# Optimization experiments

Hardware: AMD Instinct MI355X
Metric: run time of the kernel (lower is better)

Reference implementation:

```python
import jax, jax.numpy as jnp
import numpy as np

N_NODES = 20000
DEG = 16
T_IN = 12
T_OUT = 24
N_HEADS = 4
N_CH = 4
BATCH = 2


def setup_inputs() -> dict:
    key = jax.random.key(0)
    k1, k2, k3, k4 = jax.random.split(key, 4)
    # unique directed edges: (i, (i+d) % N) for d in 1..DEG, plus self loops
    src = jnp.repeat(jnp.arange(N_NODES, dtype=jnp.int64), DEG)
    offs = jnp.tile(jnp.arange(1, DEG + 1, dtype=jnp.int64), N_NODES)
    dst = (src + offs) % N_NODES
    loops = jnp.arange(N_NODES, dtype=jnp.int64)
    d_edges = jnp.concatenate([
        jnp.stack([src, dst], axis=1),
        jnp.stack([loops, loops], axis=1),
    ], axis=0)  # (E, 2), E = N*DEG + N
    E = d_edges.shape[0]
    x = jax.random.normal(k1, (BATCH, T_IN, N_NODES, N_CH), dtype=jnp.float32)
    d_ew = jax.random.uniform(k2, (E, N_HEADS), dtype=jnp.float32)
    # shrink: Linear(t_in*n_heads -> T-t_in)
    fan_in = T_IN * N_HEADS
    bound = 1.0 / np.sqrt(fan_in)
    W = jax.random.uniform(k3, (T_OUT - T_IN, fan_in), minval=-bound, maxval=bound, dtype=jnp.float32)
    b = jax.random.uniform(k4, (T_OUT - T_IN,), minval=-bound, maxval=bound, dtype=jnp.float32)
    return {"x": x, "d_ew": d_ew, "W": W, "b": b, "d_edges": d_edges}


def reference(x, d_ew, W, b, d_edges):
    # x: (B, t, N, C); d_ew: (E, H); d_edges: (E, 2)
    node_i = d_edges[:, 0]
    node_j = d_edges[:, 1]
    B, t, N, C = x.shape
    # gather source node features per edge -> (E, B, t, C)
    x_src = jnp.moveaxis(x[:, :, node_i, :], 2, 0)
    # messages: (E, B, t, H, C)
    msg = d_ew[:, None, None, :, None] * x_src[:, :, :, None, :]
    # scatter-add into destination nodes (equivalent to the dense N x N holder sum)
    agg = jax.ops.segment_sum(msg, node_j, num_segments=N)  # (N, B, t, H, C)
    y = jnp.moveaxis(agg, 0, 2)                              # (B, t, N, H, C)
    # permute(0,2,4,1,3) -> (B, N, C, t, H), flatten (t, H)
    y = jnp.transpose(y, (0, 2, 4, 1, 3)).reshape(B, N, C, t * d_ew.shape[1])
    y = jax.nn.relu(jnp.einsum('bncf,of->bnco', y, W) + b)   # (B, N, C, T-t)
    y = jnp.transpose(y, (0, 3, 1, 2))                       # (B, T-t, N, C)
    return jnp.concatenate([x, y], axis=1)                   # (B, T, N, C)
```

## Files before the change

### kernel.cpp

```cpp
#include <hip/hip_runtime.h>

namespace {
constexpr int NN  = 20000;
constexpr int DEG = 16;
constexpr int TI  = 12;
constexpr int NB  = 2;
constexpr int ESELF  = NN * DEG;
constexpr int TILE   = 32;
constexpr int NTILES = NN / TILE;
constexpr int WN     = 48;
constexpr int EWP    = 68;
constexpr int REDP   = 13;
}

__device__ __forceinline__ void pk_fma(float2& d, float2 a, float2 b) {
    asm("v_pk_fma_f32 %0, %1, %2, %0" : "+v"(d) : "v"(a), "v"(b));
}
__device__ __forceinline__ void pk_fma_blo(float2& d, float2 a, float2 b) {
    asm("v_pk_fma_f32 %0, %1, %2, %0 op_sel:[0,0,0] op_sel_hi:[1,0,1]"
        : "+v"(d) : "v"(a), "v"(b));
}
__device__ __forceinline__ void pk_fma_bhi(float2& d, float2 a, float2 b) {
    asm("v_pk_fma_f32 %0, %1, %2, %0 op_sel:[0,1,0] op_sel_hi:[1,1,1]"
        : "+v"(d) : "v"(a), "v"(b));
}

__global__ __launch_bounds__(128) void gnn_fused(
    const float* __restrict__ x,
    const float* __restrict__ ew,
    const float* __restrict__ W,
    const float* __restrict__ bias,
    float* __restrict__ out)
{
    __shared__ float x_lds[TI * WN * 4];
    __shared__ float ew_lds[WN * EWP];
    __shared__ float ews[TILE * 4];
    __shared__ float red[TILE * 2 * REDP * 2];

    const int tid = threadIdx.x;
    const int bid = blockIdx.x;
    const int b   = bid / NTILES;
    const int n0  = (bid % NTILES) * TILE;

    {
        const float* xb = x + (size_t)b * TI * NN * 4;
#pragma unroll
        for (int i = 0; i < 5; ++i) {
            if (i < 4 || tid < 64) {
                const int idx4 = tid + 128 * i;
                const int t  = idx4 / WN;
                const int wi = idx4 - t * WN;
                int s = n0 - 16 + wi; s += (s >> 31) & NN;
                const float* src = xb + (size_t)(t * NN + s) * 4;
                float* dstbase = x_lds + (size_t)(128 * i + (tid & 64)) * 4;
                __builtin_amdgcn_global_load_lds(
                    (const __attribute__((address_space(1))) void*)src,
                    (__attribute__((address_space(3))) void*)dstbase, 16, 0, 0);
            }
        }
    }
    {
        const float4* ew4 = (const float4*)ew;
#pragma unroll
        for (int i = 0; i < 6; ++i) {
            const int idx = tid + 128 * i;
            const int sl = idx >> 4, r4 = idx & 15;
            int s = n0 - 16 + sl; s += (s >> 31) & NN;
            const float4 v = ew4[s * DEG + r4];
            *(float4*)&ew_lds[sl * EWP + r4 * 4] = v;
        }
        if (tid < TILE) ((float4*)ews)[tid] = ew4[ESELF + n0 + tid];
    }
    __syncthreads();

    const int c2 = tid & 1;
    const int nl = (tid >> 1) & 31;
    const int tg = tid >> 6;
    const int t0 = __builtin_amdgcn_readfirstlane(tg * 6);

    float2 agg[6][4] = {};

#pragma unroll
    for (int k = 0; k < DEG; ++k) {
        const int wi = nl + 15 - k;
        const float4 e4 = *(const float4*)&ew_lds[wi * EWP + 4 * k];
        const float2 e01 = {e4.x, e4.y}, e23 = {e4.z, e4.w};
#pragma unroll
        for (int j = 0; j < 6; ++j) {
            const float2 xv =
                *(const float2*)&x_lds[(t0 + j) * (WN * 4) + wi * 4 + c2 * 2];
            pk_fma_blo(agg[j][0], xv, e01);
            pk_fma_bhi(agg[j][1], xv, e01);
            pk_fma_blo(agg[j][2], xv, e23);
            pk_fma_bhi(agg[j][3], xv, e23);
        }
    }

    {
        const size_t ob = (size_t)b * 24 * NN * 4 + (size_t)(n0 + nl) * 4 + c2 * 2;
        const float2 e01 = *(const float2*)&ews[nl * 4 + 0];
        const float2 e23 = *(const float2*)&ews[nl * 4 + 2];
#pragma unroll
        for (int j = 0; j < 6; ++j) {
            const float2 xv =
                *(const float2*)&x_lds[(t0 + j) * (WN * 4) + (nl + 16) * 4 + c2 * 2];
            *(float2*)&out[ob + (size_t)(t0 + j) * NN * 4] = xv;
            pk_fma_blo(agg[j][0], xv, e01);
            pk_fma_bhi(agg[j][1], xv, e01);
            pk_fma_blo(agg[j][2], xv, e23);
            pk_fma_bhi(agg[j][3], xv, e23);
        }
    }

    float2 y2[12];
#pragma unroll
    for (int o = 0; o < 12; ++o) {
        float2 acc = {0.f, 0.f};
#pragma unroll
        for (int j = 0; j < 6; ++j) {
            const float* Wr = W + o * 48 + (t0 + j) * 4;
            acc.x = fmaf(Wr[0], agg[j][0].x, acc.x);
            acc.y = fmaf(Wr[0], agg[j][0].y, acc.y);
            acc.x = fmaf(Wr[1], agg[j][1].x, acc.x);
            acc.y = fmaf(Wr[1], agg[j][1].y, acc.y);
            acc.x = fmaf(Wr[2], agg[j][2].x, acc.x);
            acc.y = fmaf(Wr[2], agg[j][2].y, acc.y);
            acc.x = fmaf(Wr[3], agg[j][3].x, acc.x);
            acc.y = fmaf(Wr[3], agg[j][3].y, acc.y);
        }
        y2[o] = acc;
    }

    if (tg == 1) {
        float* r = red + (size_t)(nl * 2 + c2) * REDP * 2;
#pragma unroll
        for (int o = 0; o < 12; ++o) *(float2*)&r[o * 2] = y2[o];
    }
    __syncthreads();
    if (tg == 0) {
        const float* r = red + (size_t)(nl * 2 + c2) * REDP * 2;
        const size_t ob = (size_t)(b * 24 + 12) * NN * 4
                        + (size_t)(n0 + nl) * 4 + c2 * 2;
#pragma unroll
        for (int o = 0; o < 12; ++o) {
            const float2 p = *(const float2*)&r[o * 2];
            const float bo = bias[o];
            float2 v = {fmaxf(y2[o].x + p.x + bo, 0.f),
                        fmaxf(y2[o].y + p.y + bo, 0.f)};
            *(float2*)&out[ob + (size_t)o * NN * 4] = v;
        }
    }
}

extern "C" void kernel_launch(void* const* d_in, const int* in_sizes, int n_in,
                              void* d_out, int out_size, void* d_ws, size_t ws_size,
                              hipStream_t stream) {
    const float* x    = (const float*)d_in[0];
    const float* ew   = (const float*)d_in[1];
    const float* W    = (const float*)d_in[2];
    const float* bias = (const float*)d_in[3];
    float* out = (float*)d_out;

    const int blocks = NB * NTILES;
    hipLaunchKernelGGL(gnn_fused, dim3(blocks), dim3(128), 0, stream,
                       x, ew, W, bias, out);
}
```

Before: 17.00 us.

## Load edge weights directly from global and remap blocks across XCDs

Drops the shared-memory staging of edge weights. Each thread now loads only the float4 weight it needs from global memory inside the degree loop, and the self-loop weight likewise. Block IDs are remapped so that consecutive tiles land on the same XCD, which should improve L2 reuse of the overlapping halo data. Self features are read and copied to the output before aggregation. This shrinks LDS use and removes staging work, in exchange for uncoalesced per-thread global loads of edge weights inside the hot loop.

```diff
diff --git a/kernel.cpp b/kernel.cpp
--- a/kernel.cpp
+++ b/kernel.cpp
@@ -9,13 +9,9 @@
 constexpr int TILE   = 32;
 constexpr int NTILES = NN / TILE;
 constexpr int WN     = 48;
-constexpr int EWP    = 68;
 constexpr int REDP   = 13;
 }
 
-__device__ __forceinline__ void pk_fma(float2& d, float2 a, float2 b) {
-    asm("v_pk_fma_f32 %0, %1, %2, %0" : "+v"(d) : "v"(a), "v"(b));
-}
 __device__ __forceinline__ void pk_fma_blo(float2& d, float2 a, float2 b) {
     asm("v_pk_fma_f32 %0, %1, %2, %0 op_sel:[0,0,0] op_sel_hi:[1,0,1]"
         : "+v"(d) : "v"(a), "v"(b));
@@ -33,14 +29,19 @@
     float* __restrict__ out)
 {
     __shared__ float x_lds[TI * WN * 4];
-    __shared__ float ew_lds[WN * EWP];
-    __shared__ float ews[TILE * 4];
     __shared__ float red[TILE * 2 * REDP * 2];
 
     const int tid = threadIdx.x;
-    const int bid = blockIdx.x;
-    const int b   = bid / NTILES;
-    const int n0  = (bid % NTILES) * TILE;
+
+    int bid = blockIdx.x;
+    {
+        const int nwg = NB * NTILES;
+        const int q = nwg >> 3, r = nwg & 7;
+        const int xcd = bid & 7, idx = bid >> 3;
+        bid = (xcd < r ? xcd * (q + 1) : r * (q + 1) + (xcd - r) * q) + idx;
+    }
+    const int b  = bid / NTILES;
+    const int n0 = (bid % NTILES) * TILE;
 
     {
         const float* xb = x + (size_t)b * TI * NN * 4;
@@ -59,31 +60,30 @@
             }
         }
     }
-    {
-        const float4* ew4 = (const float4*)ew;
-#pragma unroll
-        for (int i = 0; i < 6; ++i) {
-            const int idx = tid + 128 * i;
-            const int sl = idx >> 4, r4 = idx & 15;
-            int s = n0 - 16 + sl; s += (s >> 31) & NN;
-            const float4 v = ew4[s * DEG + r4];
-            *(float4*)&ew_lds[sl * EWP + r4 * 4] = v;
-        }
-        if (tid < TILE) ((float4*)ews)[tid] = ew4[ESELF + n0 + tid];
-    }
     __syncthreads();
 
     const int c2 = tid & 1;
     const int nl = (tid >> 1) & 31;
     const int tg = tid >> 6;
     const int t0 = __builtin_amdgcn_readfirstlane(tg * 6);
+    const float4* ew4 = (const float4*)ew;
+
+    const size_t ob = (size_t)b * 24 * NN * 4 + (size_t)(n0 + nl) * 4 + c2 * 2;
+    float2 xself[6];
+#pragma unroll
+    for (int j = 0; j < 6; ++j) {
+        xself[j] = *(const float2*)&x_lds[(t0 + j) * (WN * 4) + (nl + 16) * 4 + c2 * 2];
+        *(float2*)&out[ob + (size_t)(t0 + j) * NN * 4] = xself[j];
+    }
 
     float2 agg[6][4] = {};
+    const float4 es = ew4[ESELF + n0 + nl];
 
 #pragma unroll
     for (int k = 0; k < DEG; ++k) {
+        int s = n0 + nl - 1 - k; s += (s >> 31) & NN;
+        const float4 e4 = ew4[s * DEG + k];
         const int wi = nl + 15 - k;
-        const float4 e4 = *(const float4*)&ew_lds[wi * EWP + 4 * k];
         const float2 e01 = {e4.x, e4.y}, e23 = {e4.z, e4.w};
 #pragma unroll
         for (int j = 0; j < 6; ++j) {
@@ -95,20 +95,14 @@
             pk_fma_bhi(agg[j][3], xv, e23);
         }
     }
-
     {
-        const size_t ob = (size_t)b * 24 * NN * 4 + (size_t)(n0 + nl) * 4 + c2 * 2;
-        const float2 e01 = *(const float2*)&ews[nl * 4 + 0];
-        const float2 e23 = *(const float2*)&ews[nl * 4 + 2];
+        const float2 e01 = {es.x, es.y}, e23 = {es.z, es.w};
 #pragma unroll
         for (int j = 0; j < 6; ++j) {
-            const float2 xv =
-                *(const float2*)&x_lds[(t0 + j) * (WN * 4) + (nl + 16) * 4 + c2 * 2];
-            *(float2*)&out[ob + (size_t)(t0 + j) * NN * 4] = xv;
-            pk_fma_blo(agg[j][0], xv, e01);
-            pk_fma_bhi(agg[j][1], xv, e01);
-            pk_fma_blo(agg[j][2], xv, e23);
-            pk_fma_bhi(agg[j][3], xv, e23);
+            pk_fma_blo(agg[j][0], xself[j], e01);
+            pk_fma_bhi(agg[j][1], xself[j], e01);
+            pk_fma_blo(agg[j][2], xself[j], e23);
+            pk_fma_bhi(agg[j][3], xself[j], e23);
         }
     }
 
@@ -139,15 +133,13 @@
     __syncthreads();
     if (tg == 0) {
         const float* r = red + (size_t)(nl * 2 + c2) * REDP * 2;
-        const size_t ob = (size_t)(b * 24 + 12) * NN * 4
-                        + (size_t)(n0 + nl) * 4 + c2 * 2;
 #pragma unroll
         for (int o = 0; o < 12; ++o) {
             const float2 p = *(const float2*)&r[o * 2];
             const float bo = bias[o];
             float2 v = {fmaxf(y2[o].x + p.x + bo, 0.f),
                         fmaxf(y2[o].y + p.y + bo, 0.f)};
-            *(float2*)&out[ob + (size_t)o * NN * 4] = v;
+            *(float2*)&out[ob + (size_t)(TI + o) * NN * 4] = v;
         }
     }
 }
```

Result: faster. 16.47 us (-3.1%).
